# Kernel tuning notes

Measured on AMD Instinct MI355X. Metric: run time of the kernel, lower is better.

## Reference

```python
import jax, jax.numpy as jnp
import numpy as np


def _simple_rnn(x_tbd, Wx, Wh, b, return_sequences):
    # x_tbd: [T, B, D]; h_t = tanh(x_t @ Wx + h_{t-1} @ Wh + b)
    B = x_tbd.shape[1]
    H = Wh.shape[0]
    # precompute input projection for all steps (single big GEMM)
    xw = jnp.einsum('tbd,dh->tbh', x_tbd, Wx) + b

    def step(h, xw_t):
        h_new = jnp.tanh(xw_t + h @ Wh)
        return h_new, h_new if return_sequences else None

    h0 = jnp.zeros((B, H), dtype=x_tbd.dtype)
    h_last, hs = jax.lax.scan(step, h0, xw)
    return hs if return_sequences else h_last


def setup_inputs() -> dict:
    key = jax.random.key(0)
    ks = jax.random.split(key, 8)
    B, T, D, H, C = 32, 1024, 128, 512, 10
    s_in = 1.0 / np.sqrt(D)
    s_h = 1.0 / np.sqrt(H)
    return {
        'x': jax.random.normal(ks[0], (B, T, D), jnp.float32),
        'Wx1': jax.random.normal(ks[1], (D, H), jnp.float32) * s_in,
        'Wh1': jax.random.normal(ks[2], (H, H), jnp.float32) * s_h,
        'b1': jnp.zeros((H,), jnp.float32),
        'Wx2': jax.random.normal(ks[3], (H, H), jnp.float32) * s_h,
        'Wh2': jax.random.normal(ks[4], (H, H), jnp.float32) * s_h,
        'b2': jnp.zeros((H,), jnp.float32),
        'Wo': jax.random.normal(ks[5], (H, C), jnp.float32) * s_h,
        'bo': jnp.zeros((C,), jnp.float32),
    }


def reference(x, Wx1, Wh1, b1, Wx2, Wh2, b2, Wo, bo):
    # x: [B, T, D] -> time-major [T, B, D]
    x_t = jnp.swapaxes(x, 0, 1)
    h1 = _simple_rnn(x_t, Wx1, Wh1, b1, return_sequences=True)   # [T, B, H]
    h2 = _simple_rnn(h1, Wx2, Wh2, b2, return_sequences=False)   # [B, H]
    logits = h2 @ Wo + bo
    return jax.nn.softmax(logits, axis=-1)
```

## Files before the change

kernel.cpp:

```cpp
#include <hip/hip_runtime.h>
#include <hip/hip_fp16.h>
#include <math.h>

#define BATCH 32
#define TLEN  1024
#define DIN   128
#define HID   512
#define NCLS  10
#define SENT64 0xFFFFFFFFFFFFFFFFull
#define POLL_CAP (1u<<17)
#define PADR 68

typedef _Float16 hf2 __attribute__((ext_vector_type(2)));

__device__ __forceinline__ unsigned long long aload64(const unsigned long long* p) {
  return __hip_atomic_load(p, __ATOMIC_RELAXED, __HIP_MEMORY_SCOPE_AGENT);
}
__device__ __forceinline__ void astore64(unsigned long long* p, unsigned long long v) {
  __hip_atomic_store(p, v, __ATOMIC_RELAXED, __HIP_MEMORY_SCOPE_AGENT);
}

__device__ __forceinline__ float fdot2u(unsigned a, unsigned b, float c) {
#if __has_builtin(__builtin_amdgcn_fdot2)
  return __builtin_amdgcn_fdot2(__builtin_bit_cast(hf2, a),
                                __builtin_bit_cast(hf2, b), c, false);
#else
  hf2 av = __builtin_bit_cast(hf2, a), bv = __builtin_bit_cast(hf2, b);
  return c + (float)av[0] * (float)bv[0] + (float)av[1] * (float)bv[1];
#endif
}
__device__ __forceinline__ unsigned packh2(float lo, float hi) {
  __half2 h = __floats2half2_rn(lo, hi);
  return __builtin_bit_cast(unsigned, h);
}
__device__ __forceinline__ float f16of(unsigned u, int hi) {
  hf2 v = __builtin_bit_cast(hf2, u);
  return (float)v[hi];
}

__global__ __launch_bounds__(512) void k_prep(
    const float* __restrict__ Wh1, const float* __restrict__ Wx2,
    const float* __restrict__ Wh2, uint4* __restrict__ wcol3)
{
  const int r = blockIdx.x >> 4;
  const int s = blockIdx.x & 15;
  const int tid = threadIdx.x;
  const int w = tid >> 6, l = tid & 63, q = l >> 4, lo = l & 15;
  const int col3 = 4 * (w * 16 + lo) + 3;
  const int k0 = q * 128;
  const float* W = (r == 0) ? Wh1 : ((r == 1) ? Wx2 : Wh2);
  unsigned vv[4];
#pragma unroll
  for (int j = 0; j < 4; ++j) {
    const int k = k0 + 2 * (4 * s + j);
    vv[j] = packh2(W[(size_t)k * HID + col3], W[(size_t)(k + 1) * HID + col3]);
  }
  wcol3[((size_t)r * 16 + s) * 512 + tid] = make_uint4(vv[0], vv[1], vv[2], vv[3]);
}

__global__ __launch_bounds__(256) void k_xw1(
    const float* __restrict__ x, const float* __restrict__ Wx1,
    const float* __restrict__ b1, unsigned* __restrict__ xw1)
{
  __shared__ float xst[DIN * 4];
  const int tid  = threadIdx.x;
  const int row0 = blockIdx.x * 4;
  for (int idx = tid; idx < 4 * DIN; idx += 256) {
    int r = idx >> 7, d = idx & (DIN - 1);
    int row = row0 + r;
    int t = row >> 5, b = row & 31;
    xst[d * 4 + r] = x[((size_t)b * TLEN + t) * DIN + d];
  }
  __syncthreads();
  float acc[4][2];
#pragma unroll
  for (int r = 0; r < 4; ++r) { acc[r][0] = 0.f; acc[r][1] = 0.f; }
  const int j0 = 2 * tid, j1 = 2 * tid + 1;
  for (int d = 0; d < DIN; ++d) {
    float w0 = Wx1[(size_t)d * HID + j0];
    float w1 = Wx1[(size_t)d * HID + j1];
    float4 xv = *reinterpret_cast<const float4*>(&xst[d * 4]);
    acc[0][0] += xv.x * w0; acc[0][1] += xv.x * w1;
    acc[1][0] += xv.y * w0; acc[1][1] += xv.y * w1;
    acc[2][0] += xv.z * w0; acc[2][1] += xv.z * w1;
    acc[3][0] += xv.w * w0; acc[3][1] += xv.w * w1;
  }
  float bb0 = b1[j0], bb1 = b1[j1];
#pragma unroll
  for (int r = 0; r < 4; ++r)
    xw1[(size_t)(row0 + r) * 256 + tid] = packh2(acc[r][0] + bb0, acc[r][1] + bb1);
}

__global__ __launch_bounds__(512)
__attribute__((amdgpu_waves_per_eu(2, 2)))
void k_rnn(
    const unsigned* __restrict__ xw1,
    const float* __restrict__ Wh1, const float* __restrict__ Wx2,
    const float* __restrict__ Wh2, const float* __restrict__ b2,
    const uint4* __restrict__ wcol3,
    unsigned long long* __restrict__ h1f,
    unsigned long long* __restrict__ xw2f,
    float* __restrict__ h2fin)
{
  const int tid  = threadIdx.x;
  const int wgid = blockIdx.x;
  const int role = wgid >> 5;
  const int b    = wgid & 31;
  const int w  = tid >> 6, l = tid & 63;
  const int q  = l >> 4;
  const int lo = l & 15;
  const int cb = 4 * (w * 16 + lo);
  const int k0 = q * 128;

  __shared__ __align__(16) uint4 wl_s[16][512];
  __shared__ __align__(16) unsigned h_s[2][4 * PADR];

  for (int idx = tid; idx < 2 * 4 * PADR; idx += 512)
    ((unsigned*)h_s)[idx] = 0u;

  {
    const uint4* wp = wcol3 + (size_t)role * 16 * 512 + tid;
#pragma unroll
    for (int s = 0; s < 16; ++s) wl_s[s][tid] = wp[(size_t)s * 512];
  }
  const float* WS = (role == 0) ? Wh1 : ((role == 1) ? Wx2 : Wh2);
  unsigned w0[64], w1[64], w2[64];
#pragma unroll
  for (int i = 0; i < 16; ++i) {
    const int rr = 4 * ((i + q) & 15);
#pragma unroll
    for (int j = 0; j < 4; ++j) {
      const int k = k0 + 2 * (rr + j);
      const float *r0 = &WS[(size_t)k * HID + cb], *r1 = &WS[(size_t)(k + 1) * HID + cb];
      w0[4 * i + j] = packh2(r0[0], r1[0]);
      w1[4 * i + j] = packh2(r0[1], r1[1]);
      w2[4 * i + j] = packh2(r0[2], r1[2]);
    }
  }
  float4 b2v = make_float4(0.f, 0.f, 0.f, 0.f);
  if (role == 1 && q == 0) b2v = *reinterpret_cast<const float4*>(&b2[cb]);

  const int sgA = cb >> 1;
  const int padA = (sgA >> 6) * PADR + (sgA & 63);
  const int sgB = 2 * tid;
  const int padB = (sgB >> 6) * PADR + (sgB & 63);

  unsigned long long hu = 0;
  __syncthreads();

  for (int t = 0; t < TLEN; ++t) {
    const int p = t & 1;
    unsigned long long xv = 0;
    const unsigned long long* cprobe = nullptr;

    if (role == 0) {
      if (q == 0) {
        if (t > 0) *(unsigned long long*)&h_s[p][padA] = hu;
        xv = *(const unsigned long long*)&xw1[((size_t)t * BATCH + b) * 256 + (cb >> 1)];
      }
    } else if (role == 1) {
      if (tid < 128) {
        const unsigned long long* ph = &h1f[((size_t)t * BATCH + b) * 128 + tid];
        unsigned long long pv = aload64(ph);
        unsigned it = 0;
        while (pv == SENT64 && ++it < POLL_CAP) pv = aload64(ph);
        if (pv == SENT64) pv = 0;
        *(unsigned long long*)&h_s[p][padB] = pv;
      }
    } else {
      if (q == 0) {
        if (t > 0) *(unsigned long long*)&h_s[p][padA] = hu;
        cprobe = &xw2f[((size_t)t * BATCH + b) * 128 + (w * 16 + lo)];
        xv = aload64(cprobe);
      }
    }

    __syncthreads();

    if (role == 0 && q == 0 && t > 0)
      astore64(&h1f[((size_t)(t - 1) * BATCH + b) * 128 + (w * 16 + lo)], hu);
    if (role == 1 && q == 0 && t > 0)
      astore64(&xw2f[((size_t)(t - 1) * BATCH + b) * 128 + (w * 16 + lo)], hu);

    float a0 = 0.f, a1 = 0.f, a2 = 0.f, a3 = 0.f;
#pragma unroll
    for (int i = 0; i < 16; ++i) {
      const int sidx = (i + q) & 15;
      uint4 hv = *reinterpret_cast<const uint4*>(&h_s[p][q * PADR + 4 * sidx]);
      uint4 c3 = wl_s[sidx][tid];
      a0 = fdot2u(hv.x, w0[4 * i + 0], a0);
      a0 = fdot2u(hv.y, w0[4 * i + 1], a0);
      a0 = fdot2u(hv.z, w0[4 * i + 2], a0);
      a0 = fdot2u(hv.w, w0[4 * i + 3], a0);
      a1 = fdot2u(hv.x, w1[4 * i + 0], a1);
      a1 = fdot2u(hv.y, w1[4 * i + 1], a1);
      a1 = fdot2u(hv.z, w1[4 * i + 2], a1);
      a1 = fdot2u(hv.w, w1[4 * i + 3], a1);
      a2 = fdot2u(hv.x, w2[4 * i + 0], a2);
      a2 = fdot2u(hv.y, w2[4 * i + 1], a2);
      a2 = fdot2u(hv.z, w2[4 * i + 2], a2);
      a2 = fdot2u(hv.w, w2[4 * i + 3], a2);
      a3 = fdot2u(hv.x, c3.x, a3);
      a3 = fdot2u(hv.y, c3.y, a3);
      a3 = fdot2u(hv.z, c3.z, a3);
      a3 = fdot2u(hv.w, c3.w, a3);
    }
    a0 += __shfl_xor(a0, 16); a0 += __shfl_xor(a0, 32);
    a1 += __shfl_xor(a1, 16); a1 += __shfl_xor(a1, 32);
    a2 += __shfl_xor(a2, 16); a2 += __shfl_xor(a2, 32);
    a3 += __shfl_xor(a3, 16); a3 += __shfl_xor(a3, 32);

    if (q == 0) {
      if (role == 0) {
        unsigned xl = (unsigned)xv, xh = (unsigned)(xv >> 32);
        float h0v = tanhf(a0 + f16of(xl, 0));
        float h1v = tanhf(a1 + f16of(xl, 1));
        float h2v = tanhf(a2 + f16of(xh, 0));
        float h3v = tanhf(a3 + f16of(xh, 1));
        hu = ((unsigned long long)packh2(h2v, h3v) << 32) | packh2(h0v, h1v);
      } else if (role == 1) {
        hu = ((unsigned long long)packh2(a2 + b2v.z, a3 + b2v.w) << 32)
             | packh2(a0 + b2v.x, a1 + b2v.y);
      } else {
        if (xv == SENT64) {
          unsigned it = 0;
          do { xv = aload64(cprobe); } while (xv == SENT64 && ++it < POLL_CAP);
          if (xv == SENT64) xv = 0;
        }
        unsigned xl = (unsigned)xv, xh = (unsigned)(xv >> 32);
        float h0v = tanhf(a0 + f16of(xl, 0));
        float h1v = tanhf(a1 + f16of(xl, 1));
        float h2v = tanhf(a2 + f16of(xh, 0));
        float h3v = tanhf(a3 + f16of(xh, 1));
        hu = ((unsigned long long)packh2(h2v, h3v) << 32) | packh2(h0v, h1v);
        if (t == TLEN - 1)
          *reinterpret_cast<float4*>(&h2fin[(size_t)b * HID + cb]) =
              make_float4(h0v, h1v, h2v, h3v);
      }
    }
  }
  if (role == 0 && q == 0)
    astore64(&h1f[((size_t)(TLEN - 1) * BATCH + b) * 128 + (w * 16 + lo)], hu);
  if (role == 1 && q == 0)
    astore64(&xw2f[((size_t)(TLEN - 1) * BATCH + b) * 128 + (w * 16 + lo)], hu);
}

__global__ __launch_bounds__(640) void k_head(
    const float* __restrict__ h2, const float* __restrict__ Wo,
    const float* __restrict__ bo, float* __restrict__ out)
{
  __shared__ float lg[16];
  const int b = blockIdx.x;
  const int c = threadIdx.x >> 6;
  const int l = threadIdx.x & 63;
  float p = 0.f;
#pragma unroll
  for (int i = 0; i < 8; ++i) {
    int k = l + 64 * i;
    p += h2[(size_t)b * HID + k] * Wo[(size_t)k * NCLS + c];
  }
  for (int off = 32; off; off >>= 1) p += __shfl_down(p, off);
  if (l == 0) lg[c] = p + bo[c];
  __syncthreads();
  if (threadIdx.x == 0) {
    float m = lg[0];
    for (int i = 1; i < NCLS; ++i) m = fmaxf(m, lg[i]);
    float e[NCLS];
    float s = 0.f;
    for (int i = 0; i < NCLS; ++i) { e[i] = expf(lg[i] - m); s += e[i]; }
    for (int i = 0; i < NCLS; ++i) out[(size_t)b * NCLS + i] = e[i] / s;
  }
}

extern "C" void kernel_launch(void* const* d_in, const int* in_sizes, int n_in,
                              void* d_out, int out_size, void* d_ws, size_t ws_size,
                              hipStream_t stream)
{
  (void)in_sizes; (void)n_in; (void)out_size; (void)ws_size;
  const float* x   = (const float*)d_in[0];
  const float* Wx1 = (const float*)d_in[1];
  const float* Wh1 = (const float*)d_in[2];
  const float* b1  = (const float*)d_in[3];
  const float* Wx2 = (const float*)d_in[4];
  const float* Wh2 = (const float*)d_in[5];
  const float* b2  = (const float*)d_in[6];
  const float* Wo  = (const float*)d_in[7];
  const float* bo  = (const float*)d_in[8];
  float* out = (float*)d_out;

  char* ws = (char*)d_ws;
  size_t o = 0;
  unsigned* xw1 = (unsigned*)(ws + o);              o += (size_t)TLEN * BATCH * 256 * 4;
  unsigned long long* h1f  = (unsigned long long*)(ws + o); o += (size_t)TLEN * BATCH * 128 * 8;
  unsigned long long* xw2f = (unsigned long long*)(ws + o); o += (size_t)TLEN * BATCH * 128 * 8;
  uint4* wcol3 = (uint4*)(ws + o);                  o += (size_t)3 * 16 * 512 * 16;
  float* h2fin = (float*)(ws + o);                  o += (size_t)BATCH * HID * 4;

  hipMemsetAsync(h1f, 0xFF, (size_t)2 * TLEN * BATCH * 128 * 8, stream);

  k_prep<<<48, 512, 0, stream>>>(Wh1, Wx2, Wh2, wcol3);
  k_xw1<<<TLEN * BATCH / 4, 256, 0, stream>>>(x, Wx1, b1, xw1);
  k_rnn<<<96, 512, 0, stream>>>(xw1, Wh1, Wx2, Wh2, b2, wcol3, h1f, xw2f, h2fin);
  k_head<<<BATCH, 640, 0, stream>>>(h2fin, Wo, bo, out);
}
```

Before: 2.453 ms.

## Retile recurrent matvec to 8 columns per thread with 8-way K split

Each thread now computes 8 output columns over a 64-element K slice instead of 4 columns over 128, so a single shared-memory h read feeds 8 dot products. The cross-lane reduction drops from a 4-way to an 8-way shuffle tree. Six columns of weights stay in registers and two in LDS. The weights are now packed directly inside the RNN kernel, which removes the prep kernel and its workspace. The input projection is staged in shared memory and polled cooperatively by 128 threads, taking the consumer poll off the post-compute critical path. The tradeoff is more register pressure (48 uint4) and a longer shuffle reduction.

```diff
diff --git a/kernel.cpp b/kernel.cpp
--- a/kernel.cpp
+++ b/kernel.cpp
@@ -9,7 +9,7 @@
 #define NCLS  10
 #define SENT64 0xFFFFFFFFFFFFFFFFull
 #define POLL_CAP (1u<<17)
-#define PADR 68
+#define HP 36
 
 typedef _Float16 hf2 __attribute__((ext_vector_type(2)));
 
@@ -36,26 +36,6 @@
 __device__ __forceinline__ float f16of(unsigned u, int hi) {
   hf2 v = __builtin_bit_cast(hf2, u);
   return (float)v[hi];
-}
-
-__global__ __launch_bounds__(512) void k_prep(
-    const float* __restrict__ Wh1, const float* __restrict__ Wx2,
-    const float* __restrict__ Wh2, uint4* __restrict__ wcol3)
-{
-  const int r = blockIdx.x >> 4;
-  const int s = blockIdx.x & 15;
-  const int tid = threadIdx.x;
-  const int w = tid >> 6, l = tid & 63, q = l >> 4, lo = l & 15;
-  const int col3 = 4 * (w * 16 + lo) + 3;
-  const int k0 = q * 128;
-  const float* W = (r == 0) ? Wh1 : ((r == 1) ? Wx2 : Wh2);
-  unsigned vv[4];
-#pragma unroll
-  for (int j = 0; j < 4; ++j) {
-    const int k = k0 + 2 * (4 * s + j);
-    vv[j] = packh2(W[(size_t)k * HID + col3], W[(size_t)(k + 1) * HID + col3]);
-  }
-  wcol3[((size_t)r * 16 + s) * 512 + tid] = make_uint4(vv[0], vv[1], vv[2], vv[3]);
 }
 
 __global__ __launch_bounds__(256) void k_xw1(
@@ -91,13 +71,12 @@
     xw1[(size_t)(row0 + r) * 256 + tid] = packh2(acc[r][0] + bb0, acc[r][1] + bb1);
 }
 
-__global__ __launch_bounds__(512)
+__global__ __attribute__((amdgpu_flat_work_group_size(512, 512)))
 __attribute__((amdgpu_waves_per_eu(2, 2)))
 void k_rnn(
     const unsigned* __restrict__ xw1,
     const float* __restrict__ Wh1, const float* __restrict__ Wx2,
     const float* __restrict__ Wh2, const float* __restrict__ b2,
-    const uint4* __restrict__ wcol3,
     unsigned long long* __restrict__ h1f,
     unsigned long long* __restrict__ xw2f,
     float* __restrict__ h2fin)
@@ -107,56 +86,67 @@
   const int role = wgid >> 5;
   const int b    = wgid & 31;
   const int w  = tid >> 6, l = tid & 63;
-  const int q  = l >> 4;
-  const int lo = l & 15;
-  const int cb = 4 * (w * 16 + lo);
-  const int k0 = q * 128;
+  const int kg = l & 7;
+  const int cg = w * 8 + (l >> 3);
+  const int cb = 8 * cg;
+  const int k0 = kg * 64;
 
   __shared__ __align__(16) uint4 wl_s[16][512];
-  __shared__ __align__(16) unsigned h_s[2][4 * PADR];
-
-  for (int idx = tid; idx < 2 * 4 * PADR; idx += 512)
-    ((unsigned*)h_s)[idx] = 0u;
-
-  {
-    const uint4* wp = wcol3 + (size_t)role * 16 * 512 + tid;
-#pragma unroll
-    for (int s = 0; s < 16; ++s) wl_s[s][tid] = wp[(size_t)s * 512];
-  }
+  __shared__ __align__(16) unsigned h_s[2][8 * HP];
+  __shared__ __align__(16) unsigned xw_s[2][8 * HP];
+
+  for (int idx = tid; idx < 2 * 8 * HP; idx += 512) {
+    h_s[0][idx >= 8 * HP ? idx - 8 * HP : idx] = 0u;
+    if (idx < 8 * HP) h_s[1][idx] = 0u;
+  }
+
   const float* WS = (role == 0) ? Wh1 : ((role == 1) ? Wx2 : Wh2);
-  unsigned w0[64], w1[64], w2[64];
-#pragma unroll
-  for (int i = 0; i < 16; ++i) {
-    const int rr = 4 * ((i + q) & 15);
-#pragma unroll
-    for (int j = 0; j < 4; ++j) {
-      const int k = k0 + 2 * (rr + j);
-      const float *r0 = &WS[(size_t)k * HID + cb], *r1 = &WS[(size_t)(k + 1) * HID + cb];
-      w0[4 * i + j] = packh2(r0[0], r1[0]);
-      w1[4 * i + j] = packh2(r0[1], r1[1]);
-      w2[4 * i + j] = packh2(r0[2], r1[2]);
-    }
-  }
-  float4 b2v = make_float4(0.f, 0.f, 0.f, 0.f);
-  if (role == 1 && q == 0) b2v = *reinterpret_cast<const float4*>(&b2[cb]);
-
-  const int sgA = cb >> 1;
-  const int padA = (sgA >> 6) * PADR + (sgA & 63);
-  const int sgB = 2 * tid;
-  const int padB = (sgB >> 6) * PADR + (sgB & 63);
-
-  unsigned long long hu = 0;
+  uint4 wr[48];
+#pragma unroll
+  for (int c = 0; c < 6; ++c) {
+#pragma unroll
+    for (int j = 0; j < 8; ++j) {
+      const int col = cb + c, k = k0 + 8 * j;
+      wr[c * 8 + j] = make_uint4(
+          packh2(WS[(size_t)(k + 0) * HID + col], WS[(size_t)(k + 1) * HID + col]),
+          packh2(WS[(size_t)(k + 2) * HID + col], WS[(size_t)(k + 3) * HID + col]),
+          packh2(WS[(size_t)(k + 4) * HID + col], WS[(size_t)(k + 5) * HID + col]),
+          packh2(WS[(size_t)(k + 6) * HID + col], WS[(size_t)(k + 7) * HID + col]));
+    }
+  }
+#pragma unroll
+  for (int c = 0; c < 2; ++c) {
+#pragma unroll
+    for (int j = 0; j < 8; ++j) {
+      const int col = cb + 6 + c, k = k0 + 8 * j;
+      wl_s[c * 8 + j][tid] = make_uint4(
+          packh2(WS[(size_t)(k + 0) * HID + col], WS[(size_t)(k + 1) * HID + col]),
+          packh2(WS[(size_t)(k + 2) * HID + col], WS[(size_t)(k + 3) * HID + col]),
+          packh2(WS[(size_t)(k + 4) * HID + col], WS[(size_t)(k + 5) * HID + col]),
+          packh2(WS[(size_t)(k + 6) * HID + col], WS[(size_t)(k + 7) * HID + col]));
+    }
+  }
+  float4 b2lo = make_float4(0.f, 0.f, 0.f, 0.f), b2hi = b2lo;
+  if (role == 1 && kg == 0) {
+    b2lo = *reinterpret_cast<const float4*>(&b2[cb]);
+    b2hi = *reinterpret_cast<const float4*>(&b2[cb + 4]);
+  }
+
+  const int padO = (cg >> 3) * HP + ((4 * cg) & 31);
+  const int padS = (tid >> 4) * HP + ((2 * tid) & 31);
+
+  uint4 huv = make_uint4(0, 0, 0, 0);
   __syncthreads();
 
   for (int t = 0; t < TLEN; ++t) {
     const int p = t & 1;
-    unsigned long long xv = 0;
-    const unsigned long long* cprobe = nullptr;
 
     if (role == 0) {
-      if (q == 0) {
-        if (t > 0) *(unsigned long long*)&h_s[p][padA] = hu;
-        xv = *(const unsigned long long*)&xw1[((size_t)t * BATCH + b) * 256 + (cb >> 1)];
+      if (kg == 0 && t > 0) *(uint4*)&h_s[p][padO] = huv;
+      if (tid < 128) {
+        unsigned long long xv =
+            *(const unsigned long long*)&xw1[((size_t)t * BATCH + b) * 256 + 2 * tid];
+        *(unsigned long long*)&xw_s[p][padS] = xv;
       }
     } else if (role == 1) {
       if (tid < 128) {
@@ -165,84 +155,100 @@
         unsigned it = 0;
         while (pv == SENT64 && ++it < POLL_CAP) pv = aload64(ph);
         if (pv == SENT64) pv = 0;
-        *(unsigned long long*)&h_s[p][padB] = pv;
+        *(unsigned long long*)&h_s[p][padS] = pv;
       }
     } else {
-      if (q == 0) {
-        if (t > 0) *(unsigned long long*)&h_s[p][padA] = hu;
-        cprobe = &xw2f[((size_t)t * BATCH + b) * 128 + (w * 16 + lo)];
-        xv = aload64(cprobe);
+      if (kg == 0 && t > 0) *(uint4*)&h_s[p][padO] = huv;
+      if (tid < 128) {
+        const unsigned long long* ph = &xw2f[((size_t)t * BATCH + b) * 128 + tid];
+        unsigned long long pv = aload64(ph);
+        unsigned it = 0;
+        while (pv == SENT64 && ++it < POLL_CAP) pv = aload64(ph);
+        if (pv == SENT64) pv = 0;
+        *(unsigned long long*)&xw_s[p][padS] = pv;
       }
     }
 
     __syncthreads();
 
-    if (role == 0 && q == 0 && t > 0)
-      astore64(&h1f[((size_t)(t - 1) * BATCH + b) * 128 + (w * 16 + lo)], hu);
-    if (role == 1 && q == 0 && t > 0)
-      astore64(&xw2f[((size_t)(t - 1) * BATCH + b) * 128 + (w * 16 + lo)], hu);
-
-    float a0 = 0.f, a1 = 0.f, a2 = 0.f, a3 = 0.f;
-#pragma unroll
-    for (int i = 0; i < 16; ++i) {
-      const int sidx = (i + q) & 15;
-      uint4 hv = *reinterpret_cast<const uint4*>(&h_s[p][q * PADR + 4 * sidx]);
-      uint4 c3 = wl_s[sidx][tid];
-      a0 = fdot2u(hv.x, w0[4 * i + 0], a0);
-      a0 = fdot2u(hv.y, w0[4 * i + 1], a0);
-      a0 = fdot2u(hv.z, w0[4 * i + 2], a0);
-      a0 = fdot2u(hv.w, w0[4 * i + 3], a0);
-      a1 = fdot2u(hv.x, w1[4 * i + 0], a1);
-      a1 = fdot2u(hv.y, w1[4 * i + 1], a1);
-      a1 = fdot2u(hv.z, w1[4 * i + 2], a1);
-      a1 = fdot2u(hv.w, w1[4 * i + 3], a1);
-      a2 = fdot2u(hv.x, w2[4 * i + 0], a2);
-      a2 = fdot2u(hv.y, w2[4 * i + 1], a2);
-      a2 = fdot2u(hv.z, w2[4 * i + 2], a2);
-      a2 = fdot2u(hv.w, w2[4 * i + 3], a2);
-      a3 = fdot2u(hv.x, c3.x, a3);
-      a3 = fdot2u(hv.y, c3.y, a3);
-      a3 = fdot2u(hv.z, c3.z, a3);
-      a3 = fdot2u(hv.w, c3.w, a3);
-    }
-    a0 += __shfl_xor(a0, 16); a0 += __shfl_xor(a0, 32);
-    a1 += __shfl_xor(a1, 16); a1 += __shfl_xor(a1, 32);
-    a2 += __shfl_xor(a2, 16); a2 += __shfl_xor(a2, 32);
-    a3 += __shfl_xor(a3, 16); a3 += __shfl_xor(a3, 32);
-
-    if (q == 0) {
+    if (kg == 0 && t > 0) {
+      unsigned long long u0 = ((unsigned long long)huv.y << 32) | huv.x;
+      unsigned long long u1 = ((unsigned long long)huv.w << 32) | huv.z;
       if (role == 0) {
-        unsigned xl = (unsigned)xv, xh = (unsigned)(xv >> 32);
-        float h0v = tanhf(a0 + f16of(xl, 0));
-        float h1v = tanhf(a1 + f16of(xl, 1));
-        float h2v = tanhf(a2 + f16of(xh, 0));
-        float h3v = tanhf(a3 + f16of(xh, 1));
-        hu = ((unsigned long long)packh2(h2v, h3v) << 32) | packh2(h0v, h1v);
+        astore64(&h1f[((size_t)(t - 1) * BATCH + b) * 128 + 2 * cg], u0);
+        astore64(&h1f[((size_t)(t - 1) * BATCH + b) * 128 + 2 * cg + 1], u1);
       } else if (role == 1) {
-        hu = ((unsigned long long)packh2(a2 + b2v.z, a3 + b2v.w) << 32)
-             | packh2(a0 + b2v.x, a1 + b2v.y);
+        astore64(&xw2f[((size_t)(t - 1) * BATCH + b) * 128 + 2 * cg], u0);
+        astore64(&xw2f[((size_t)(t - 1) * BATCH + b) * 128 + 2 * cg + 1], u1);
+      }
+    }
+
+    float acc[8];
+#pragma unroll
+    for (int c = 0; c < 8; ++c) acc[c] = 0.f;
+#pragma unroll
+    for (int j = 0; j < 8; ++j) {
+      uint4 hv = *reinterpret_cast<const uint4*>(&h_s[p][kg * HP + 4 * j]);
+#pragma unroll
+      for (int c = 0; c < 6; ++c) {
+        uint4 wv = wr[c * 8 + j];
+        acc[c] = fdot2u(hv.x, wv.x, acc[c]);
+        acc[c] = fdot2u(hv.y, wv.y, acc[c]);
+        acc[c] = fdot2u(hv.z, wv.z, acc[c]);
+        acc[c] = fdot2u(hv.w, wv.w, acc[c]);
+      }
+      uint4 c6 = wl_s[j][tid];
+      uint4 c7 = wl_s[8 + j][tid];
+      acc[6] = fdot2u(hv.x, c6.x, acc[6]);
+      acc[6] = fdot2u(hv.y, c6.y, acc[6]);
+      acc[6] = fdot2u(hv.z, c6.z, acc[6]);
+      acc[6] = fdot2u(hv.w, c6.w, acc[6]);
+      acc[7] = fdot2u(hv.x, c7.x, acc[7]);
+      acc[7] = fdot2u(hv.y, c7.y, acc[7]);
+      acc[7] = fdot2u(hv.z, c7.z, acc[7]);
+      acc[7] = fdot2u(hv.w, c7.w, acc[7]);
+    }
+#pragma unroll
+    for (int c = 0; c < 8; ++c) {
+      acc[c] += __shfl_xor(acc[c], 1);
+      acc[c] += __shfl_xor(acc[c], 2);
+      acc[c] += __shfl_xor(acc[c], 4);
+    }
+
+    if (kg == 0) {
+      if (role == 1) {
+        huv = make_uint4(packh2(acc[0] + b2lo.x, acc[1] + b2lo.y),
+                         packh2(acc[2] + b2lo.z, acc[3] + b2lo.w),
+                         packh2(acc[4] + b2hi.x, acc[5] + b2hi.y),
+                         packh2(acc[6] + b2hi.z, acc[7] + b2hi.w));
       } else {
-        if (xv == SENT64) {
-          unsigned it = 0;
-          do { xv = aload64(cprobe); } while (xv == SENT64 && ++it < POLL_CAP);
-          if (xv == SENT64) xv = 0;
+        uint4 xv4 = *reinterpret_cast<const uint4*>(&xw_s[p][padO]);
+        float h0 = tanhf(acc[0] + f16of(xv4.x, 0));
+        float h1 = tanhf(acc[1] + f16of(xv4.x, 1));
+        float h2 = tanhf(acc[2] + f16of(xv4.y, 0));
+        float h3 = tanhf(acc[3] + f16of(xv4.y, 1));
+        float h4 = tanhf(acc[4] + f16of(xv4.z, 0));
+        float h5 = tanhf(acc[5] + f16of(xv4.z, 1));
+        float h6 = tanhf(acc[6] + f16of(xv4.w, 0));
+        float h7 = tanhf(acc[7] + f16of(xv4.w, 1));
+        huv = make_uint4(packh2(h0, h1), packh2(h2, h3),
+                         packh2(h4, h5), packh2(h6, h7));
+        if (role == 2 && t == TLEN - 1) {
+          *reinterpret_cast<float4*>(&h2fin[(size_t)b * HID + cb]) =
+              make_float4(h0, h1, h2, h3);
+          *reinterpret_cast<float4*>(&h2fin[(size_t)b * HID + cb + 4]) =
+              make_float4(h4, h5, h6, h7);
         }
-        unsigned xl = (unsigned)xv, xh = (unsigned)(xv >> 32);
-        float h0v = tanhf(a0 + f16of(xl, 0));
-        float h1v = tanhf(a1 + f16of(xl, 1));
-        float h2v = tanhf(a2 + f16of(xh, 0));
-        float h3v = tanhf(a3 + f16of(xh, 1));
-        hu = ((unsigned long long)packh2(h2v, h3v) << 32) | packh2(h0v, h1v);
-        if (t == TLEN - 1)
-          *reinterpret_cast<float4*>(&h2fin[(size_t)b * HID + cb]) =
-              make_float4(h0v, h1v, h2v, h3v);
-      }
-    }
-  }
-  if (role == 0 && q == 0)
-    astore64(&h1f[((size_t)(TLEN - 1) * BATCH + b) * 128 + (w * 16 + lo)], hu);
-  if (role == 1 && q == 0)
-    astore64(&xw2f[((size_t)(TLEN - 1) * BATCH + b) * 128 + (w * 16 + lo)], hu);
+      }
+    }
+  }
+  if (kg == 0 && role != 2) {
+    unsigned long long u0 = ((unsigned long long)huv.y << 32) | huv.x;
+    unsigned long long u1 = ((unsigned long long)huv.w << 32) | huv.z;
+    unsigned long long* dst = (role == 0) ? h1f : xw2f;
+    astore64(&dst[((size_t)(TLEN - 1) * BATCH + b) * 128 + 2 * cg], u0);
+    astore64(&dst[((size_t)(TLEN - 1) * BATCH + b) * 128 + 2 * cg + 1], u1);
+  }
 }
 
 __global__ __launch_bounds__(640) void k_head(
@@ -293,13 +299,11 @@
   unsigned* xw1 = (unsigned*)(ws + o);              o += (size_t)TLEN * BATCH * 256 * 4;
   unsigned long long* h1f  = (unsigned long long*)(ws + o); o += (size_t)TLEN * BATCH * 128 * 8;
   unsigned long long* xw2f = (unsigned long long*)(ws + o); o += (size_t)TLEN * BATCH * 128 * 8;
-  uint4* wcol3 = (uint4*)(ws + o);                  o += (size_t)3 * 16 * 512 * 16;
   float* h2fin = (float*)(ws + o);                  o += (size_t)BATCH * HID * 4;
 
   hipMemsetAsync(h1f, 0xFF, (size_t)2 * TLEN * BATCH * 128 * 8, stream);
 
-  k_prep<<<48, 512, 0, stream>>>(Wh1, Wx2, Wh2, wcol3);
   k_xw1<<<TLEN * BATCH / 4, 256, 0, stream>>>(x, Wx1, b1, xw1);
-  k_rnn<<<96, 512, 0, stream>>>(xw1, Wh1, Wx2, Wh2, b2, wcol3, h1f, xw2f, h2fin);
+  k_rnn<<<96, 512, 0, stream>>>(xw1, Wh1, Wx2, Wh2, b2, h1f, xw2f, h2fin);
   k_head<<<BATCH, 640, 0, stream>>>(h2fin, Wo, bo, out);
 }
```

Result: slower. 2.757 ms (+12.4%).
